# Kernel optimization log

Measured on AMD Instinct MI355X. Metric: run time of the kernel, lower is better.

Reference implementation:

```python
import jax, jax.numpy as jnp
import numpy as np

NUM_LAYERS = 12        # architecture layers to sample
NUM_BRANCHES = 8       # choices per layer (w_emb vocab)
LSTM_SIZE = 1024
LSTM_NUM_LAYERS = 2
TEMPERATURE = 5.0
TANH_CONSTANT = 2.5
NUM_STEPS = NUM_LAYERS * NUM_BRANCHES  # 96 sequential decisions


def setup_inputs() -> dict:
    key = jax.random.key(0)
    ks = jax.random.split(key, 7)
    s = 0.1  # nn.init.uniform_(-0.1, 0.1)
    L = LSTM_SIZE
    u = lambda k, shape: jax.random.uniform(k, shape, jnp.float32, -s, s)
    return {
        "g_emb_w": u(ks[0], (1, L)),                          # Embedding(1, L)
        "w_emb_w": u(ks[1], (NUM_BRANCHES, L)),               # Embedding(num_branches, L)
        "w_soft_w": u(ks[2], (2, L)),                         # Linear(L, 2, bias=False)
        "w_ih": u(ks[3], (LSTM_NUM_LAYERS, 4 * L, L)),        # per-layer W_ih (i,f,g,o)
        "w_hh": u(ks[4], (LSTM_NUM_LAYERS, 4 * L, L)),        # per-layer W_hh
        "b_ih": u(ks[5], (LSTM_NUM_LAYERS, 4 * L)),
        "b_hh": u(ks[6], (LSTM_NUM_LAYERS, 4 * L)),
    }


def _lstm_cells(x, h, c, w_ih, w_hh, b_ih, b_hh):
    """One time-step through the stacked LSTM. x: [L], h/c: [n_layers, L]."""
    hs, cs = [], []
    inp = x
    for l in range(LSTM_NUM_LAYERS):  # fixed, structurally distinct layers
        gates = w_ih[l] @ inp + b_ih[l] + w_hh[l] @ h[l] + b_hh[l]  # [4L]
        i, f, g, o = jnp.split(gates, 4)  # PyTorch gate order i,f,g,o
        c_new = jax.nn.sigmoid(f) * c[l] + jax.nn.sigmoid(i) * jnp.tanh(g)
        h_new = jax.nn.sigmoid(o) * jnp.tanh(c_new)
        hs.append(h_new)
        cs.append(c_new)
        inp = h_new
    return inp, jnp.stack(hs), jnp.stack(cs)


def reference(g_emb_w, w_emb_w, w_soft_w, w_ih, w_hh, b_ih, b_hh):
    L = LSTM_SIZE
    keys = jax.random.split(jax.random.key(42), NUM_STEPS)

    def step(carry, k):
        x, h, c = carry
        out, h, c = _lstm_cells(x, h, c, w_ih, w_hh, b_ih, b_hh)
        logit = TANH_CONSTANT * jnp.tanh((w_soft_w @ out) / TEMPERATURE)  # [2]
        logp = jax.nn.log_softmax(logit)
        sample = jax.random.categorical(k, logit)          # on-device categorical
        log_prob = logp[sample]
        entropy = -jnp.sum(jnp.exp(logp) * logp)
        x_next = w_emb_w[sample]                           # embedding feedback
        return (x_next, h, c), (sample, log_prob, entropy)

    zeros = jnp.zeros((LSTM_NUM_LAYERS, L), g_emb_w.dtype)
    init = (g_emb_w[0], zeros, zeros)
    _, (arc_seq, log_probs, entropies) = jax.lax.scan(step, init, keys)
    return arc_seq, jnp.sum(entropies), jnp.sum(log_probs)
```

## Files before the change

### kernel.cpp

```cpp
#include <hip/hip_runtime.h>
#include <cstdint>
#include <cstddef>

#define NSTEPS 96
#define HID 1024
#define NBLK 256
#define NTHR 512

#define BUFSZ 3584
#define H1OFF 0
#define H0COFF 1024
#define POFF 3072
#define WS_FLAGS 7168
#define WS_TOTAL 15360

#define PIN4(v) asm volatile("" : "+v"(v.x), "+v"(v.y), "+v"(v.z), "+v"(v.w))

__device__ __forceinline__ float ld_llc(const float* p) {
  return __hip_atomic_load(p, __ATOMIC_RELAXED, __HIP_MEMORY_SCOPE_AGENT);
}
__device__ __forceinline__ void st_llc(float* p, float v) {
  __hip_atomic_store(p, v, __ATOMIC_RELAXED, __HIP_MEMORY_SCOPE_AGENT);
}

__device__ __forceinline__ void tf2x32(uint32_t k0, uint32_t k1,
                                       uint32_t x0, uint32_t x1,
                                       uint32_t& o0, uint32_t& o1) {
  uint32_t ks[3] = {k0, k1, k0 ^ k1 ^ 0x1BD11BDAu};
  x0 += ks[0];
  x1 += ks[1];
  const uint32_t R[2][4] = {{13u, 15u, 26u, 6u}, {17u, 29u, 16u, 24u}};
#pragma unroll
  for (int i = 0; i < 5; ++i) {
#pragma unroll
    for (int r = 0; r < 4; ++r) {
      uint32_t rot = R[i & 1][r];
      x0 += x1;
      x1 = (x1 << rot) | (x1 >> (32u - rot));
      x1 ^= x0;
    }
    x0 += ks[(i + 1) % 3];
    x1 += ks[(i + 2) % 3] + (uint32_t)(i + 1);
  }
  o0 = x0;
  o1 = x1;
}

__device__ __forceinline__ float jax_uniform(uint32_t bits) {
  const float TINY = 1.17549435e-38f;
  float f = __uint_as_float((bits >> 9) | 0x3f800000u) - 1.0f;
  f = f * (1.0f - TINY) + TINY;
  return fmaxf(TINY, f);
}

__device__ __forceinline__ float sigmoidf_(float x) {
  return 1.0f / (1.0f + expf(-x));
}

__global__ void __launch_bounds__(NTHR, 1)
enas_controller(const float* __restrict__ g_emb,
                const float* __restrict__ w_emb,
                const float* __restrict__ w_soft,
                const float* __restrict__ w_ih,
                const float* __restrict__ w_hh,
                const float* __restrict__ b_ih,
                const float* __restrict__ b_hh,
                float* __restrict__ out,
                float* __restrict__ ws) {
  const int tid = threadIdx.x;
  const int b = blockIdx.x;
  const int row_idx = tid >> 5;
  const int sub = tid & 31;
  const int q = row_idx >> 2;
  const int j = row_idx & 3;
  const int row = q * HID + (b * 4 + j);
  const int col0 = sub * 4;

  float* flags = ws + WS_FLAGS;

  __shared__ __align__(16) float hxS[3 * HID];
  __shared__ float xdotPre[16][3];
  __shared__ float bsumS[2][16];
  __shared__ float wsoftS[2][4];
  __shared__ float gatesS[16];
  __shared__ float hdotS[16];
  __shared__ float cS1[4];
  __shared__ float c0cand[2][4];
  __shared__ float hS[4];
  __shared__ float wredS[2][8];
  __shared__ int sampS;

  float4 Wih1[8], Whh1[8], Whh0[8];
  {
    const float* p_ih1 = w_ih + (size_t)(4096 + row) * HID;
    const float* p_hh0 = w_hh + (size_t)row * HID;
    const float* p_hh1 = w_hh + (size_t)(4096 + row) * HID;
#pragma unroll
    for (int i = 0; i < 8; ++i) {
      Wih1[i] = *(const float4*)(p_ih1 + col0 + i * 128);
      Whh0[i] = *(const float4*)(p_hh0 + col0 + i * 128);
      Whh1[i] = *(const float4*)(p_hh1 + col0 + i * 128);
    }
#pragma unroll
    for (int i = 0; i < 8; ++i) { PIN4(Wih1[i]); PIN4(Whh0[i]); PIN4(Whh1[i]); }
  }
  {
    const float* p_ih0 = w_ih + (size_t)row * HID;
    const float* xs[3] = {w_emb, w_emb + HID, g_emb};
#pragma unroll
    for (int vi = 0; vi < 3; ++vi) {
      float a = 0.0f;
#pragma unroll
      for (int i = 0; i < 8; ++i) {
        float4 wv = *(const float4*)(p_ih0 + col0 + i * 128);
        float4 xv = *(const float4*)(xs[vi] + col0 + i * 128);
        a = fmaf(wv.x, xv.x, a); a = fmaf(wv.y, xv.y, a);
        a = fmaf(wv.z, xv.z, a); a = fmaf(wv.w, xv.w, a);
      }
#pragma unroll
      for (int m = 16; m >= 1; m >>= 1) a += __shfl_xor(a, m, 64);
      if (sub == 0) xdotPre[row_idx][vi] = a;
    }
    if (tid < 32) {
      int l = tid >> 4, r = tid & 15;
      int rw = (r >> 2) * HID + b * 4 + (r & 3);
      bsumS[l][r] = b_ih[l * 4096 + rw] + b_hh[l * 4096 + rw];
    }
    if (tid < 8) wsoftS[tid >> 2][tid & 3] = w_soft[(tid >> 2) * HID + b * 4 + (tid & 3)];
    if (tid < 4) cS1[tid] = 0.0f;
  }
  __syncthreads();

  {
    float* bufW = ws;
    if (tid < 4) {
      float gi = xdotPre[tid][2] + bsumS[0][tid];
      float gg = xdotPre[8 + tid][2] + bsumS[0][8 + tid];
      float go = xdotPre[12 + tid][2] + bsumS[0][12 + tid];
      float cn = sigmoidf_(gi) * tanhf(gg);
      float hn = sigmoidf_(go) * tanhf(cn);
      c0cand[0][tid] = cn;
      c0cand[1][tid] = cn;
      st_llc(&bufW[H0COFF + b * 4 + tid], hn);
      st_llc(&bufW[H0COFF + HID + b * 4 + tid], hn);
    }
    __syncthreads();
    if (tid == 0) {
      asm volatile("s_waitcnt vmcnt(0)" ::: "memory");
      st_llc(&flags[b * 32], __uint_as_float(1u));
    }
  }

  float accE = 0.0f, accLP = 0.0f;

  for (int k = 0; k <= NSTEPS; ++k) {
    {
      const unsigned e = (unsigned)(k + 1);
      int ok;
      do {
        unsigned f = e;
        if (tid < NBLK)
          f = __float_as_uint(ld_llc(&flags[tid * 32]));
        ok = (f >= e);
      } while (!__syncthreads_and(ok));
      asm volatile("" ::: "memory");
    }

    const float* bufR = ws + (size_t)(k & 1) * BUFSZ;
    float* bufW = ws + (size_t)((k + 1) & 1) * BUFSZ;

    {
      float stg[6];
#pragma unroll
      for (int w = 0; w < 6; ++w) stg[w] = ld_llc(&bufR[w * NTHR + tid]);
#pragma unroll
      for (int w = 0; w < 6; ++w) hxS[w * NTHR + tid] = stg[w];
    }
    float v0 = 0.0f, v1 = 0.0f;
    if (k > 0 && tid < NBLK) {
      v0 = ld_llc(&bufR[POFF + tid]);
      v1 = ld_llc(&bufR[POFF + NBLK + tid]);
    }
    __syncthreads();

    const float* h1v = hxS;
    const float* h0c0 = hxS + HID;
    const float* h0c1 = hxS + 2 * HID;
    float aW1c0 = 0.0f, aW1c1 = 0.0f, aH0c0 = 0.0f, aH0c1 = 0.0f, aHH1 = 0.0f;
#pragma unroll
    for (int i = 0; i < 8; ++i) {
      float4 x0 = *(const float4*)(h0c0 + col0 + i * 128);
      float4 x1 = *(const float4*)(h0c1 + col0 + i * 128);
      float4 hh = *(const float4*)(h1v + col0 + i * 128);
      aW1c0 = fmaf(Wih1[i].x, x0.x, aW1c0); aW1c0 = fmaf(Wih1[i].y, x0.y, aW1c0);
      aW1c0 = fmaf(Wih1[i].z, x0.z, aW1c0); aW1c0 = fmaf(Wih1[i].w, x0.w, aW1c0);
      aW1c1 = fmaf(Wih1[i].x, x1.x, aW1c1); aW1c1 = fmaf(Wih1[i].y, x1.y, aW1c1);
      aW1c1 = fmaf(Wih1[i].z, x1.z, aW1c1); aW1c1 = fmaf(Wih1[i].w, x1.w, aW1c1);
      aH0c0 = fmaf(Whh0[i].x, x0.x, aH0c0); aH0c0 = fmaf(Whh0[i].y, x0.y, aH0c0);
      aH0c0 = fmaf(Whh0[i].z, x0.z, aH0c0); aH0c0 = fmaf(Whh0[i].w, x0.w, aH0c0);
      aH0c1 = fmaf(Whh0[i].x, x1.x, aH0c1); aH0c1 = fmaf(Whh0[i].y, x1.y, aH0c1);
      aH0c1 = fmaf(Whh0[i].z, x1.z, aH0c1); aH0c1 = fmaf(Whh0[i].w, x1.w, aH0c1);
      aHH1 = fmaf(Whh1[i].x, hh.x, aHH1); aHH1 = fmaf(Whh1[i].y, hh.y, aHH1);
      aHH1 = fmaf(Whh1[i].z, hh.z, aHH1); aHH1 = fmaf(Whh1[i].w, hh.w, aHH1);
    }

    int smp = 0;
    if (k > 0) {
#pragma unroll
      for (int m = 32; m >= 1; m >>= 1) {
        v0 += __shfl_xor(v0, m, 64);
        v1 += __shfl_xor(v1, m, 64);
      }
      if ((tid & 63) == 0) {
        wredS[0][tid >> 6] = v0;
        wredS[1][tid >> 6] = v1;
      }
      __syncthreads();
      if (tid == 0) {
        float t0 = ((wredS[0][0] + wredS[0][1]) + (wredS[0][2] + wredS[0][3])) +
                   ((wredS[0][4] + wredS[0][5]) + (wredS[0][6] + wredS[0][7]));
        float t1 = ((wredS[1][0] + wredS[1][1]) + (wredS[1][2] + wredS[1][3])) +
                   ((wredS[1][4] + wredS[1][5]) + (wredS[1][6] + wredS[1][7]));
        float l0 = 2.5f * tanhf(t0 / 5.0f);
        float l1 = 2.5f * tanhf(t1 / 5.0f);
        float m = fmaxf(l0, l1);
        float s0 = l0 - m, s1 = l1 - m;
        float lse = logf(expf(s0) + expf(s1));
        float lp0 = s0 - lse, lp1 = s1 - lse;
        uint32_t sk0, sk1, bt0, bt1, a, c;
        tf2x32(0u, 42u, 0u, (uint32_t)(k - 1), sk0, sk1);
        tf2x32(sk0, sk1, 0u, 0u, a, c); bt0 = a ^ c;
        tf2x32(sk0, sk1, 0u, 1u, a, c); bt1 = a ^ c;
        float gum0 = -logf(-logf(jax_uniform(bt0)));
        float gum1 = -logf(-logf(jax_uniform(bt1)));
        int sm = (gum1 + l1 > gum0 + l0) ? 1 : 0;
        accE += -(expf(lp0) * lp0 + expf(lp1) * lp1);
        accLP += sm ? lp1 : lp0;
        sampS = sm;
        if (b == 0) out[k - 1] = (float)sm;
      }
      __syncthreads();
      smp = sampS;
    }
    if (k == NSTEPS) break;

    float a1 = (smp ? aW1c1 : aW1c0) + aHH1;
    float a0 = smp ? aH0c1 : aH0c0;
#pragma unroll
    for (int m = 16; m >= 1; m >>= 1) {
      a1 += __shfl_xor(a1, m, 64);
      a0 += __shfl_xor(a0, m, 64);
    }
    if (sub == 0) {
      gatesS[row_idx] = a1 + bsumS[1][row_idx];
      hdotS[row_idx] = a0;
    }
    __syncthreads();

    if (tid < 4) {
      {
        float gi = gatesS[tid], gf = gatesS[4 + tid];
        float gg = gatesS[8 + tid], go = gatesS[12 + tid];
        float c = cS1[tid];
        float cn = sigmoidf_(gf) * c + sigmoidf_(gi) * tanhf(gg);
        float hn = sigmoidf_(go) * tanhf(cn);
        cS1[tid] = cn;
        hS[tid] = hn;
        st_llc(&bufW[H1OFF + b * 4 + tid], hn);
      }
      float c0sel = c0cand[smp][tid];
#pragma unroll
      for (int jj = 0; jj < 2; ++jj) {
        float gi = xdotPre[tid][jj] + hdotS[tid] + bsumS[0][tid];
        float gf = xdotPre[4 + tid][jj] + hdotS[4 + tid] + bsumS[0][4 + tid];
        float gg = xdotPre[8 + tid][jj] + hdotS[8 + tid] + bsumS[0][8 + tid];
        float go = xdotPre[12 + tid][jj] + hdotS[12 + tid] + bsumS[0][12 + tid];
        float cn = sigmoidf_(gf) * c0sel + sigmoidf_(gi) * tanhf(gg);
        float hn = sigmoidf_(go) * tanhf(cn);
        c0cand[jj][tid] = cn;
        st_llc(&bufW[H0COFF + (size_t)jj * HID + b * 4 + tid], hn);
      }
      if (tid == 0) {
        float p0 = wsoftS[0][0] * hS[0] + wsoftS[0][1] * hS[1] +
                   wsoftS[0][2] * hS[2] + wsoftS[0][3] * hS[3];
        float p1 = wsoftS[1][0] * hS[0] + wsoftS[1][1] * hS[1] +
                   wsoftS[1][2] * hS[2] + wsoftS[1][3] * hS[3];
        st_llc(&bufW[POFF + b], p0);
        st_llc(&bufW[POFF + NBLK + b], p1);
      }
    }
    __syncthreads();
    if (tid == 0) {
      asm volatile("s_waitcnt vmcnt(0)" ::: "memory");
      st_llc(&flags[b * 32], __uint_as_float((unsigned)(k + 2)));
    }
  }

  if (b == 0 && tid == 0) {
    out[96] = accE;
    out[97] = accLP;
  }
}

extern "C" void kernel_launch(void* const* d_in, const int* in_sizes, int n_in,
                              void* d_out, int out_size, void* d_ws, size_t ws_size,
                              hipStream_t stream) {
  const float* g_emb = (const float*)d_in[0];
  const float* w_emb = (const float*)d_in[1];
  const float* w_soft = (const float*)d_in[2];
  const float* w_ih = (const float*)d_in[3];
  const float* w_hh = (const float*)d_in[4];
  const float* b_ih = (const float*)d_in[5];
  const float* b_hh = (const float*)d_in[6];
  float* out = (float*)d_out;
  float* ws = (float*)d_ws;

  hipMemsetAsync(ws, 0, WS_TOTAL * sizeof(float), stream);

  enas_controller<<<dim3(NBLK), dim3(NTHR), 0, stream>>>(
      g_emb, w_emb, w_soft, w_ih, w_hh, b_ih, b_hh, out, ws);
}
```

Measured before the change: 716.6 us.

## Shorten per-step critical path: precompute Gumbel noise, single-wave flag poll, fewer barriers

Precomputes all 96 Gumbel noise pairs into shared memory at kernel start, so the threefry hashing and logs leave the per-step serial path. The flag poll now runs on a single wavefront with __all instead of a block-wide __syncthreads_and loop. The logit reduction is done in one wave, and both gate dot products are reduced for the two sample choices before the sample is known. This removes two block barriers per step, the gate cells run on 12 threads in parallel, the flag is published before the entropy bookkeeping, and the final sample is handled after the loop by block 0. The cost is extra shuffle reductions and shared memory, plus more complex ordering between the flag store and the hS reads.

```diff
diff --git a/kernel.cpp b/kernel.cpp
--- a/kernel.cpp
+++ b/kernel.cpp
@@ -79,16 +79,14 @@
   float* flags = ws + WS_FLAGS;
 
   __shared__ __align__(16) float hxS[3 * HID];
+  __shared__ float gumS[2 * NSTEPS];
   __shared__ float xdotPre[16][3];
   __shared__ float bsumS[2][16];
   __shared__ float wsoftS[2][4];
-  __shared__ float gatesS[16];
-  __shared__ float hdotS[16];
+  __shared__ float dotS[16][4];
   __shared__ float cS1[4];
   __shared__ float c0cand[2][4];
   __shared__ float hS[4];
-  __shared__ float wredS[2][8];
-  __shared__ int sampS;
 
   float4 Wih1[8], Whh1[8], Whh0[8];
   {
@@ -120,6 +118,14 @@
 #pragma unroll
       for (int m = 16; m >= 1; m >>= 1) a += __shfl_xor(a, m, 64);
       if (sub == 0) xdotPre[row_idx][vi] = a;
+    }
+    if (tid < 96) {
+      uint32_t sk0, sk1, a, c, b0, b1;
+      tf2x32(0u, 42u, 0u, (uint32_t)tid, sk0, sk1);
+      tf2x32(sk0, sk1, 0u, 0u, a, c); b0 = a ^ c;
+      tf2x32(sk0, sk1, 0u, 1u, a, c); b1 = a ^ c;
+      gumS[2 * tid] = -logf(-logf(jax_uniform(b0)));
+      gumS[2 * tid + 1] = -logf(-logf(jax_uniform(b1)));
     }
     if (tid < 32) {
       int l = tid >> 4, r = tid & 15;
@@ -153,34 +159,38 @@
 
   float accE = 0.0f, accLP = 0.0f;
 
-  for (int k = 0; k <= NSTEPS; ++k) {
+  for (int k = 0; k < NSTEPS; ++k) {
     {
       const unsigned e = (unsigned)(k + 1);
-      int ok;
-      do {
-        unsigned f = e;
-        if (tid < NBLK)
-          f = __float_as_uint(ld_llc(&flags[tid * 32]));
-        ok = (f >= e);
-      } while (!__syncthreads_and(ok));
+      if (tid < 64) {
+        int ok;
+        do {
+          ok = 1;
+#pragma unroll
+          for (int t = 0; t < 4; ++t)
+            ok &= (__float_as_uint(ld_llc(&flags[(tid + t * 64) * 32])) >= e);
+        } while (!__all(ok));
+      }
+      __syncthreads();
       asm volatile("" ::: "memory");
     }
 
     const float* bufR = ws + (size_t)(k & 1) * BUFSZ;
     float* bufW = ws + (size_t)((k + 1) & 1) * BUFSZ;
 
-    {
-      float stg[6];
-#pragma unroll
-      for (int w = 0; w < 6; ++w) stg[w] = ld_llc(&bufR[w * NTHR + tid]);
-#pragma unroll
-      for (int w = 0; w < 6; ++w) hxS[w * NTHR + tid] = stg[w];
-    }
-    float v0 = 0.0f, v1 = 0.0f;
-    if (k > 0 && tid < NBLK) {
-      v0 = ld_llc(&bufR[POFF + tid]);
-      v1 = ld_llc(&bufR[POFF + NBLK + tid]);
-    }
+    float stg[6];
+#pragma unroll
+    for (int w = 0; w < 6; ++w) stg[w] = ld_llc(&bufR[w * NTHR + tid]);
+    float pv0[4], pv1[4];
+    if (tid < 64) {
+#pragma unroll
+      for (int t = 0; t < 4; ++t) {
+        pv0[t] = ld_llc(&bufR[POFF + tid + t * 64]);
+        pv1[t] = ld_llc(&bufR[POFF + NBLK + tid + t * 64]);
+      }
+    }
+#pragma unroll
+    for (int w = 0; w < 6; ++w) hxS[w * NTHR + tid] = stg[w];
     __syncthreads();
 
     const float* h1v = hxS;
@@ -203,102 +213,124 @@
       aHH1 = fmaf(Whh1[i].x, hh.x, aHH1); aHH1 = fmaf(Whh1[i].y, hh.y, aHH1);
       aHH1 = fmaf(Whh1[i].z, hh.z, aHH1); aHH1 = fmaf(Whh1[i].w, hh.w, aHH1);
     }
-
-    int smp = 0;
-    if (k > 0) {
+#pragma unroll
+    for (int m = 16; m >= 1; m >>= 1) {
+      aW1c0 += __shfl_xor(aW1c0, m, 64);
+      aW1c1 += __shfl_xor(aW1c1, m, 64);
+      aH0c0 += __shfl_xor(aH0c0, m, 64);
+      aH0c1 += __shfl_xor(aH0c1, m, 64);
+      aHH1 += __shfl_xor(aHH1, m, 64);
+    }
+    if (sub == 0) {
+      float gb = bsumS[1][row_idx];
+      dotS[row_idx][0] = aW1c0 + aHH1 + gb;
+      dotS[row_idx][1] = aW1c1 + aHH1 + gb;
+      dotS[row_idx][2] = aH0c0;
+      dotS[row_idx][3] = aH0c1;
+    }
+
+    int sm = 0;
+    float l0 = 0.0f, l1 = 0.0f;
+    if (tid < 64 && k > 0) {
+      float v0 = (pv0[0] + pv0[1]) + (pv0[2] + pv0[3]);
+      float v1 = (pv1[0] + pv1[1]) + (pv1[2] + pv1[3]);
 #pragma unroll
       for (int m = 32; m >= 1; m >>= 1) {
         v0 += __shfl_xor(v0, m, 64);
         v1 += __shfl_xor(v1, m, 64);
       }
-      if ((tid & 63) == 0) {
-        wredS[0][tid >> 6] = v0;
-        wredS[1][tid >> 6] = v1;
-      }
-      __syncthreads();
       if (tid == 0) {
-        float t0 = ((wredS[0][0] + wredS[0][1]) + (wredS[0][2] + wredS[0][3])) +
-                   ((wredS[0][4] + wredS[0][5]) + (wredS[0][6] + wredS[0][7]));
-        float t1 = ((wredS[1][0] + wredS[1][1]) + (wredS[1][2] + wredS[1][3])) +
-                   ((wredS[1][4] + wredS[1][5]) + (wredS[1][6] + wredS[1][7]));
-        float l0 = 2.5f * tanhf(t0 / 5.0f);
-        float l1 = 2.5f * tanhf(t1 / 5.0f);
-        float m = fmaxf(l0, l1);
-        float s0 = l0 - m, s1 = l1 - m;
+        l0 = 2.5f * tanhf(v0 / 5.0f);
+        l1 = 2.5f * tanhf(v1 / 5.0f);
+        sm = (gumS[2 * (k - 1) + 1] + l1 > gumS[2 * (k - 1)] + l0) ? 1 : 0;
+        if (b == 0) out[k - 1] = (float)sm;
+      }
+      sm = __shfl(sm, 0, 64);
+    }
+    __syncthreads();
+
+    if (tid < 12) {
+      const int cell = tid >> 2, t = tid & 3;
+      if (cell == 0) {
+        float gi = dotS[t][sm], gf = dotS[4 + t][sm];
+        float gg = dotS[8 + t][sm], go = dotS[12 + t][sm];
+        float c = cS1[t];
+        float cn = sigmoidf_(gf) * c + sigmoidf_(gi) * tanhf(gg);
+        float hn = sigmoidf_(go) * tanhf(cn);
+        cS1[t] = cn;
+        hS[t] = hn;
+        st_llc(&bufW[H1OFF + b * 4 + t], hn);
+      } else {
+        const int jj = cell - 1;
+        float gi = xdotPre[t][jj] + dotS[t][2 + sm] + bsumS[0][t];
+        float gf = xdotPre[4 + t][jj] + dotS[4 + t][2 + sm] + bsumS[0][4 + t];
+        float gg = xdotPre[8 + t][jj] + dotS[8 + t][2 + sm] + bsumS[0][8 + t];
+        float go = xdotPre[12 + t][jj] + dotS[12 + t][2 + sm] + bsumS[0][12 + t];
+        float c0sel = c0cand[sm][t];
+        float cn = sigmoidf_(gf) * c0sel + sigmoidf_(gi) * tanhf(gg);
+        float hn = sigmoidf_(go) * tanhf(cn);
+        c0cand[jj][t] = cn;
+        st_llc(&bufW[H0COFF + (size_t)jj * HID + b * 4 + t], hn);
+      }
+    }
+    if (tid == 0) {
+      float p0 = wsoftS[0][0] * hS[0] + wsoftS[0][1] * hS[1] +
+                 wsoftS[0][2] * hS[2] + wsoftS[0][3] * hS[3];
+      float p1 = wsoftS[1][0] * hS[0] + wsoftS[1][1] * hS[1] +
+                 wsoftS[1][2] * hS[2] + wsoftS[1][3] * hS[3];
+      st_llc(&bufW[POFF + b], p0);
+      st_llc(&bufW[POFF + NBLK + b], p1);
+      asm volatile("s_waitcnt vmcnt(0)" ::: "memory");
+      st_llc(&flags[b * 32], __uint_as_float((unsigned)(k + 2)));
+      if (b == 0 && k > 0) {
+        float mm = fmaxf(l0, l1);
+        float s0 = l0 - mm, s1 = l1 - mm;
         float lse = logf(expf(s0) + expf(s1));
         float lp0 = s0 - lse, lp1 = s1 - lse;
-        uint32_t sk0, sk1, bt0, bt1, a, c;
-        tf2x32(0u, 42u, 0u, (uint32_t)(k - 1), sk0, sk1);
-        tf2x32(sk0, sk1, 0u, 0u, a, c); bt0 = a ^ c;
-        tf2x32(sk0, sk1, 0u, 1u, a, c); bt1 = a ^ c;
-        float gum0 = -logf(-logf(jax_uniform(bt0)));
-        float gum1 = -logf(-logf(jax_uniform(bt1)));
-        int sm = (gum1 + l1 > gum0 + l0) ? 1 : 0;
         accE += -(expf(lp0) * lp0 + expf(lp1) * lp1);
         accLP += sm ? lp1 : lp0;
-        sampS = sm;
-        if (b == 0) out[k - 1] = (float)sm;
-      }
-      __syncthreads();
-      smp = sampS;
-    }
-    if (k == NSTEPS) break;
-
-    float a1 = (smp ? aW1c1 : aW1c0) + aHH1;
-    float a0 = smp ? aH0c1 : aH0c0;
-#pragma unroll
-    for (int m = 16; m >= 1; m >>= 1) {
-      a1 += __shfl_xor(a1, m, 64);
-      a0 += __shfl_xor(a0, m, 64);
-    }
-    if (sub == 0) {
-      gatesS[row_idx] = a1 + bsumS[1][row_idx];
-      hdotS[row_idx] = a0;
-    }
-    __syncthreads();
-
-    if (tid < 4) {
-      {
-        float gi = gatesS[tid], gf = gatesS[4 + tid];
-        float gg = gatesS[8 + tid], go = gatesS[12 + tid];
-        float c = cS1[tid];
-        float cn = sigmoidf_(gf) * c + sigmoidf_(gi) * tanhf(gg);
-        float hn = sigmoidf_(go) * tanhf(cn);
-        cS1[tid] = cn;
-        hS[tid] = hn;
-        st_llc(&bufW[H1OFF + b * 4 + tid], hn);
-      }
-      float c0sel = c0cand[smp][tid];
-#pragma unroll
-      for (int jj = 0; jj < 2; ++jj) {
-        float gi = xdotPre[tid][jj] + hdotS[tid] + bsumS[0][tid];
-        float gf = xdotPre[4 + tid][jj] + hdotS[4 + tid] + bsumS[0][4 + tid];
-        float gg = xdotPre[8 + tid][jj] + hdotS[8 + tid] + bsumS[0][8 + tid];
-        float go = xdotPre[12 + tid][jj] + hdotS[12 + tid] + bsumS[0][12 + tid];
-        float cn = sigmoidf_(gf) * c0sel + sigmoidf_(gi) * tanhf(gg);
-        float hn = sigmoidf_(go) * tanhf(cn);
-        c0cand[jj][tid] = cn;
-        st_llc(&bufW[H0COFF + (size_t)jj * HID + b * 4 + tid], hn);
-      }
-      if (tid == 0) {
-        float p0 = wsoftS[0][0] * hS[0] + wsoftS[0][1] * hS[1] +
-                   wsoftS[0][2] * hS[2] + wsoftS[0][3] * hS[3];
-        float p1 = wsoftS[1][0] * hS[0] + wsoftS[1][1] * hS[1] +
-                   wsoftS[1][2] * hS[2] + wsoftS[1][3] * hS[3];
-        st_llc(&bufW[POFF + b], p0);
-        st_llc(&bufW[POFF + NBLK + b], p1);
-      }
-    }
-    __syncthreads();
+      }
+    }
+  }
+
+  if (b == 0 && tid < 64) {
+    const unsigned e = (unsigned)(NSTEPS + 1);
+    int ok;
+    do {
+      ok = 1;
+#pragma unroll
+      for (int t = 0; t < 4; ++t)
+        ok &= (__float_as_uint(ld_llc(&flags[(tid + t * 64) * 32])) >= e);
+    } while (!__all(ok));
+    asm volatile("" ::: "memory");
+    const float* bufR = ws + (size_t)(NSTEPS & 1) * BUFSZ;
+    float pv0[4], pv1[4];
+#pragma unroll
+    for (int t = 0; t < 4; ++t) {
+      pv0[t] = ld_llc(&bufR[POFF + tid + t * 64]);
+      pv1[t] = ld_llc(&bufR[POFF + NBLK + tid + t * 64]);
+    }
+    float v0 = (pv0[0] + pv0[1]) + (pv0[2] + pv0[3]);
+    float v1 = (pv1[0] + pv1[1]) + (pv1[2] + pv1[3]);
+#pragma unroll
+    for (int m = 32; m >= 1; m >>= 1) {
+      v0 += __shfl_xor(v0, m, 64);
+      v1 += __shfl_xor(v1, m, 64);
+    }
     if (tid == 0) {
-      asm volatile("s_waitcnt vmcnt(0)" ::: "memory");
-      st_llc(&flags[b * 32], __uint_as_float((unsigned)(k + 2)));
-    }
-  }
-
-  if (b == 0 && tid == 0) {
-    out[96] = accE;
-    out[97] = accLP;
+      float l0 = 2.5f * tanhf(v0 / 5.0f);
+      float l1 = 2.5f * tanhf(v1 / 5.0f);
+      int sm = (gumS[2 * 95 + 1] + l1 > gumS[2 * 95] + l0) ? 1 : 0;
+      float mm = fmaxf(l0, l1);
+      float s0 = l0 - mm, s1 = l1 - mm;
+      float lse = logf(expf(s0) + expf(s1));
+      float lp0 = s0 - lse, lp1 = s1 - lse;
+      accE += -(expf(lp0) * lp0 + expf(lp1) * lp1);
+      accLP += sm ? lp1 : lp0;
+      out[95] = (float)sm;
+      out[96] = accE;
+      out[97] = accLP;
+    }
   }
 }
 
```

Measured after the change: 582.0 us. 18.8% less time.
